# Kernel tuning notes

Measured on AMD Instinct MI355X. Metric: run time of the kernel, lower is better.

## Reference

```python
import jax, jax.numpy as jnp
import numpy as np

DIM = 768
DEC = 768
B, N = 8, 4096


def setup_inputs() -> dict:
    key = jax.random.key(0)
    ks = jax.random.split(key, 7)
    s_in = DIM ** -0.5
    s_dec = DEC ** -0.5
    return {
        "x": jax.random.normal(ks[0], (B, N, DIM), dtype=jnp.float32),
        "Wq": jax.random.normal(ks[1], (DIM, DEC), dtype=jnp.float32) * s_in,
        "Wk": jax.random.normal(ks[2], (DIM, DEC), dtype=jnp.float32) * s_in,
        "Wv": jax.random.normal(ks[3], (DIM, DEC), dtype=jnp.float32) * s_in,
        "Wr": jax.random.normal(ks[4], (DEC, DEC), dtype=jnp.float32) * s_dec,
        "alpha": jax.random.normal(ks[5], (DEC,), dtype=jnp.float32),
        "beta": jax.random.normal(ks[6], (DEC,), dtype=jnp.float32),
    }


def reference(x, Wq, Wk, Wv, Wr, alpha, beta):
    # x: [b, n, dim] -> q/k/v: [b, n, d]
    q = jnp.einsum('bni,id->bnd', x, Wq)
    k = jnp.einsum('bni,id->bnd', x, Wk)
    v = jnp.einsum('bni,id->bnd', x, Wv)
    scale = q.shape[-1] ** -0.5

    # additive attention over feature dim (softmax along d, as in source)
    alpha_w = jax.nn.softmax(q * alpha * scale, axis=-1)          # [b, n, d]
    global_q = jnp.sum(q * alpha_w, axis=1)                        # [b, d]

    p = global_q[:, None, :] * k                                   # [b, n, d]
    beta_w = jax.nn.softmax(p * beta * scale, axis=-1)             # [b, n, d]
    global_k = jnp.sum(p * beta_w, axis=1)                         # [b, d]

    kv = global_k[:, None, :] * v                                  # [b, n, d]
    out = jnp.einsum('bnd,de->bne', kv, Wr) + q                    # [b, n, d]
    return out
```

## Files before the change

kernel.cpp:

```cpp
#include <hip/hip_runtime.h>
#include <stdint.h>


#define NBATCH 8
#define SEQ 4096
#define KD 768
#define ROWS (NBATCH * SEQ)
#define NT 12

typedef __bf16 bf16x8 __attribute__((ext_vector_type(8)));
typedef float f32x4 __attribute__((ext_vector_type(4)));

__device__ __forceinline__ unsigned short f2bf(float f) {
    __bf16 h = (__bf16)f;
    return __builtin_bit_cast(unsigned short, h);
}

__device__ __forceinline__ void gload16(const void* g, void* l) {
    __builtin_amdgcn_global_load_lds((const __attribute__((address_space(1))) void*)g,
                                     (__attribute__((address_space(3))) void*)l, 16, 0, 0);
}


__global__ __launch_bounds__(256) void cvt_f32_bf16x8(const float* __restrict__ src,
                                                      unsigned short* __restrict__ dst, int n8) {
    int i = blockIdx.x * 256 + threadIdx.x;
    if (i >= n8) return;
    const float4* p = (const float4*)src + (size_t)i * 2;
    float4 a = p[0], b = p[1];
    union { unsigned short s[8]; uint4 u; } t;
    t.s[0] = f2bf(a.x); t.s[1] = f2bf(a.y); t.s[2] = f2bf(a.z); t.s[3] = f2bf(a.w);
    t.s[4] = f2bf(b.x); t.s[5] = f2bf(b.y); t.s[6] = f2bf(b.z); t.s[7] = f2bf(b.w);
    ((uint4*)dst)[i] = t.u;
}

__global__ __launch_bounds__(256) void prep_w(const float* __restrict__ Wq,
                                              const float* __restrict__ Wk,
                                              const float* __restrict__ Wr,
                                              const float* __restrict__ Wv,
                                              unsigned short* __restrict__ Wcat,
                                              unsigned short* __restrict__ WrT,
                                              unsigned short* __restrict__ Wvb) {
    __shared__ float tile[32][33];
    const int z = blockIdx.z;
    const float* src = (z == 0) ? Wq : (z == 1) ? Wk : (z == 2) ? Wr : Wv;
    unsigned short* dst = (z == 0) ? Wcat : (z == 1) ? (Wcat + KD * KD) : (z == 2) ? WrT : Wvb;
    int tx = threadIdx.x & 31, tg = threadIdx.x >> 5;
    int bi = blockIdx.x * 32, bj = blockIdx.y * 32;
    if (z == 3) {
#pragma unroll
        for (int j = 0; j < 4; ++j) {
            int r = bi + tg * 4 + j;
            dst[(size_t)r * KD + bj + tx] = f2bf(src[(size_t)r * KD + bj + tx]);
        }
        return;
    }
#pragma unroll
    for (int j = 0; j < 4; ++j) {
        int r = tg * 4 + j;
        tile[r][tx] = src[(size_t)(bi + r) * KD + bj + tx];
    }
    __syncthreads();
#pragma unroll
    for (int j = 0; j < 4; ++j) {
        int r = tg * 4 + j;
        dst[(size_t)(bj + r) * KD + bi + tx] = f2bf(tile[tx][r]);
    }
}


template <int LDC, int EPI>
__device__ __forceinline__ void gemm_core(const unsigned short* __restrict__ A,
                                          const unsigned short* __restrict__ Bp,
                                          void* __restrict__ Cout,
                                          const float* __restrict__ Wqp,
                                          int m0, int n0, char* lds) {
    const int tid = threadIdx.x;
    const int lane = tid & 63, wave = tid >> 6;
    const int wr = wave >> 1, wc = wave & 1;
    const int hi = lane >> 4, lo = lane & 15;
    char* lA = lds;
    char* lB = lds + 98304;

    f32x4 acc[4][4] = {};

    const int colb = (tid * 16) & 127;
    const int row0 = tid >> 3;
    const int sc = colb ^ ((row0 & 7) << 4);
    const size_t ldb = (size_t)KD * 2;
    const char* sAg = (const char*)A + (size_t)(m0 + row0) * ldb + sc;
    const char* sBg = (const char*)Bp + (size_t)(n0 + row0) * ldb + sc;

    const int kksel = wave & 1;
    int offA[2][4], offB[2][4];
#pragma unroll
    for (int g = 0; g < 2; ++g) {
        const int kkg = kksel ^ g;
#pragma unroll
        for (int m = 0; m < 4; ++m) {
            int ra = wr * 64 + m * 16 + lo;
            int rb = wc * 64 + m * 16 + lo;
            offA[g][m] = ra * 128 + ((kkg * 64 + hi * 16) ^ ((ra & 7) << 4));
            offB[g][m] = rb * 128 + ((kkg * 64 + hi * 16) ^ ((rb & 7) << 4));
        }
    }

#define STAGE(t)                                                              \
    {                                                                         \
        const char* ga = sAg + (t) * 128;                                     \
        const char* gb = sBg + (t) * 128;                                     \
        char* dA = lA + ((t) % 3) * 32768 + tid * 16;                         \
        char* dB = lB + ((t) % 3) * 16384 + tid * 16;                         \
        gload16(ga, dA);                                                      \
        gload16(ga + 64 * ldb, dA + 8192);                                    \
        gload16(ga + 128 * ldb, dA + 16384);                                  \
        gload16(ga + 192 * ldb, dA + 24576);                                  \
        gload16(gb, dB);                                                      \
        gload16(gb + 64 * ldb, dB + 8192);                                    \
    }

    STAGE(0);
    STAGE(1);
    asm volatile("s_waitcnt vmcnt(6)" ::: "memory");
    __builtin_amdgcn_s_barrier();
    __builtin_amdgcn_sched_barrier(0);

    for (int t = 0; t < NT; ++t) {
        if (t + 2 < NT) STAGE(t + 2);
        const char* cA = lA + (t % 3) * 32768;
        const char* cB = lB + (t % 3) * 16384;
#pragma unroll
        for (int g = 0; g < 2; ++g) {
            bf16x8 af[4], bv[4];
#pragma unroll
            for (int m = 0; m < 4; ++m) af[m] = *(const bf16x8*)(cA + offA[g][m]);
#pragma unroll
            for (int n = 0; n < 4; ++n) bv[n] = *(const bf16x8*)(cB + offB[g][n]);
            __builtin_amdgcn_s_setprio(1);
#pragma unroll
            for (int m = 0; m < 4; ++m)
#pragma unroll
                for (int n = 0; n < 4; ++n)
                    acc[m][n] = __builtin_amdgcn_mfma_f32_16x16x32_bf16(af[m], bv[n],
                                                                        acc[m][n], 0, 0, 0);
            __builtin_amdgcn_s_setprio(0);
        }
        if (t + 2 < NT)
            asm volatile("s_waitcnt vmcnt(6)" ::: "memory");
        else
            asm volatile("s_waitcnt vmcnt(0)" ::: "memory");
        __builtin_amdgcn_s_barrier();
        __builtin_amdgcn_sched_barrier(0);
    }
#undef STAGE

    const int r0 = m0 + wr * 64 + hi * 4;
    const int c0 = n0 + wc * 64 + lo;
#pragma unroll
    for (int m = 0; m < 4; ++m)
#pragma unroll
        for (int n = 0; n < 4; ++n)
#pragma unroll
            for (int r = 0; r < 4; ++r) {
                int row = r0 + m * 16 + r, col = c0 + n * 16;
                size_t idx = (size_t)row * LDC + col;
                if (EPI == 1) {
                    ((float*)Cout)[idx] = acc[m][n][r];
                } else if (EPI == 2) {
                    ((unsigned short*)Cout)[idx] =
                        f2bf(acc[m][n][r] + Wqp[(size_t)col * KD + row]);
                } else {
                    ((unsigned short*)Cout)[idx] = f2bf(acc[m][n][r]);
                }
            }
}

__device__ __forceinline__ int xcd_swz(int bid, int nwg) {
    int cpx = nwg >> 3;
    return (bid & 7) * cpx + (bid >> 3);
}

__global__ __launch_bounds__(512) void gemm_qk(const unsigned short* __restrict__ xb,
                                               const unsigned short* __restrict__ Wcat,
                                               unsigned short* __restrict__ C) {
    __shared__ char lds[147456];
    int wg = xcd_swz(blockIdx.y * gridDim.x + blockIdx.x, gridDim.x * gridDim.y);
    gemm_core<1536, 0>(xb, Wcat, C, nullptr, (wg / 12) * 256, (wg % 12) * 128, lds);
}

__global__ __launch_bounds__(512) void gemm_w3(const unsigned short* __restrict__ WrS,
                                               const unsigned short* __restrict__ Wvb,
                                               const float* __restrict__ Wq,
                                               unsigned short* __restrict__ W3T) {
    __shared__ char lds[147456];
    const int b = blockIdx.z;
    gemm_core<KD, 2>(WrS + (size_t)b * (KD * KD), Wvb, W3T + (size_t)b * (KD * KD), Wq,
                     blockIdx.y * 256, blockIdx.x * 128, lds);
}

__global__ __launch_bounds__(512) void gemm_out_f32(const unsigned short* __restrict__ xb,
                                                    const unsigned short* __restrict__ W3T,
                                                    float* __restrict__ out) {
    __shared__ char lds[147456];
    int wg = xcd_swz(blockIdx.y * gridDim.x + blockIdx.x, gridDim.x * gridDim.y);
    const int by = wg / 6, bx = wg % 6;
    const unsigned short* Bp = W3T + (size_t)(by >> 4) * (KD * KD);
    gemm_core<KD, 1>(xb, Bp, out, nullptr, by * 256, bx * 128, lds);
}


#define SM_SCALE 0.03608439182435161f
#define LDQK 1536

__device__ __forceinline__ void unpack12(const unsigned short* rowp, int lane, float* q) {
    uint4 u = *(const uint4*)(rowp + lane * 8);
    uint2 v = *(const uint2*)(rowp + 512 + lane * 4);
    q[0] = __uint_as_float(u.x << 16);  q[1] = __uint_as_float(u.x & 0xffff0000u);
    q[2] = __uint_as_float(u.y << 16);  q[3] = __uint_as_float(u.y & 0xffff0000u);
    q[4] = __uint_as_float(u.z << 16);  q[5] = __uint_as_float(u.z & 0xffff0000u);
    q[6] = __uint_as_float(u.w << 16);  q[7] = __uint_as_float(u.w & 0xffff0000u);
    q[8] = __uint_as_float(v.x << 16);  q[9] = __uint_as_float(v.x & 0xffff0000u);
    q[10] = __uint_as_float(v.y << 16); q[11] = __uint_as_float(v.y & 0xffff0000u);
}

__device__ __forceinline__ void load12f(const float* base, int lane, float* o) {
    const float4* p0 = (const float4*)(base + lane * 8);
    float4 x0 = p0[0], x1 = p0[1];
    float4 x2 = *(const float4*)(base + 512 + lane * 4);
    o[0] = x0.x; o[1] = x0.y; o[2] = x0.z; o[3] = x0.w;
    o[4] = x1.x; o[5] = x1.y; o[6] = x1.z; o[7] = x1.w;
    o[8] = x2.x; o[9] = x2.y; o[10] = x2.z; o[11] = x2.w;
}

__device__ __forceinline__ void block_partial_store(float* acc, int lane, int wave,
                                                    float* part_dst) {
    __shared__ float buf[4][KD];
#pragma unroll
    for (int j = 0; j < 8; ++j) buf[wave][lane * 8 + j] = acc[j];
#pragma unroll
    for (int j = 0; j < 4; ++j) buf[wave][512 + lane * 4 + j] = acc[8 + j];
    __syncthreads();
#pragma unroll
    for (int d = threadIdx.x; d < KD; d += 256)
        part_dst[d] = buf[0][d] + buf[1][d] + buf[2][d] + buf[3][d];
}

__global__ __launch_bounds__(256) void reduce_gq_s1(const unsigned short* __restrict__ qk,
                                                    const float* __restrict__ alpha,
                                                    float* __restrict__ part) {
    const int b = blockIdx.y;
    const int lane = threadIdx.x & 63, wave = threadIdx.x >> 6;
    float al[12];
    load12f(alpha, lane, al);
    float acc[12];
#pragma unroll
    for (int j = 0; j < 12; ++j) acc[j] = 0.f;
    const int row0 = b * SEQ + blockIdx.x * 64 + wave * 16;
#pragma unroll 2
    for (int rr = 0; rr < 16; ++rr) {
        const unsigned short* rowp = qk + (size_t)(row0 + rr) * LDQK;
        float q[12], t[12];
        unpack12(rowp, lane, q);
        float mx = -1e30f;
#pragma unroll
        for (int j = 0; j < 12; ++j) { t[j] = q[j] * al[j] * SM_SCALE; mx = fmaxf(mx, t[j]); }
#pragma unroll
        for (int s = 32; s > 0; s >>= 1) mx = fmaxf(mx, __shfl_xor(mx, s));
        float sum = 0.f, e[12];
#pragma unroll
        for (int j = 0; j < 12; ++j) { e[j] = __expf(t[j] - mx); sum += e[j]; }
#pragma unroll
        for (int s = 32; s > 0; s >>= 1) sum += __shfl_xor(sum, s);
        float inv = 1.f / sum;
#pragma unroll
        for (int j = 0; j < 12; ++j) acc[j] += q[j] * e[j] * inv;
    }
    block_partial_store(acc, lane, wave, part + ((size_t)b * 64 + blockIdx.x) * KD);
}

__global__ __launch_bounds__(256) void reduce_gk_s1(const unsigned short* __restrict__ qk,
                                                    const float* __restrict__ part1,
                                                    const float* __restrict__ beta,
                                                    float* __restrict__ part) {
    __shared__ float sgq[KD];
    const int b = blockIdx.y;
    const int lane = threadIdx.x & 63, wave = threadIdx.x >> 6;
    {
        const float* p = part1 + (size_t)b * 64 * KD;
#pragma unroll
        for (int j = 0; j < 3; ++j) {
            int d = threadIdx.x + j * 256;
            float s = 0.f;
#pragma unroll 8
            for (int i = 0; i < 64; ++i) s += p[(size_t)i * KD + d];
            sgq[d] = s;
        }
    }
    __syncthreads();
    float bt[12], gv[12];
    load12f(beta, lane, bt);
#pragma unroll
    for (int j = 0; j < 8; ++j) gv[j] = sgq[lane * 8 + j];
#pragma unroll
    for (int j = 0; j < 4; ++j) gv[8 + j] = sgq[512 + lane * 4 + j];
    float acc[12];
#pragma unroll
    for (int j = 0; j < 12; ++j) acc[j] = 0.f;
    const int row0 = b * SEQ + blockIdx.x * 64 + wave * 16;
#pragma unroll 2
    for (int rr = 0; rr < 16; ++rr) {
        const unsigned short* rowp = qk + (size_t)(row0 + rr) * LDQK + KD;
        float k[12], p[12], t[12];
        unpack12(rowp, lane, k);
        float mx = -1e30f;
#pragma unroll
        for (int j = 0; j < 12; ++j) {
            p[j] = gv[j] * k[j];
            t[j] = p[j] * bt[j] * SM_SCALE;
            mx = fmaxf(mx, t[j]);
        }
#pragma unroll
        for (int s = 32; s > 0; s >>= 1) mx = fmaxf(mx, __shfl_xor(mx, s));
        float sum = 0.f, e[12];
#pragma unroll
        for (int j = 0; j < 12; ++j) { e[j] = __expf(t[j] - mx); sum += e[j]; }
#pragma unroll
        for (int s = 32; s > 0; s >>= 1) sum += __shfl_xor(sum, s);
        float inv = 1.f / sum;
#pragma unroll
        for (int j = 0; j < 12; ++j) acc[j] += p[j] * e[j] * inv;
    }
    block_partial_store(acc, lane, wave, part + ((size_t)b * 64 + blockIdx.x) * KD);
}

__global__ __launch_bounds__(256) void sum_scale(const float* __restrict__ part2,
                                                 const unsigned short* __restrict__ WrT,
                                                 unsigned short* __restrict__ WrS) {
    __shared__ float sgk[KD];
    const int b = blockIdx.y;
    {
        const float* p = part2 + (size_t)b * 64 * KD;
#pragma unroll
        for (int j = 0; j < 3; ++j) {
            int d = threadIdx.x + j * 256;
            float s = 0.f;
#pragma unroll 8
            for (int i = 0; i < 64; ++i) s += p[(size_t)i * KD + d];
            sgk[d] = s;
        }
    }
    __syncthreads();
    const int e0 = blockIdx.x * 32;
    unsigned short* dst = WrS + (size_t)b * (KD * KD);
#pragma unroll
    for (int c = 0; c < 12; ++c) {
        int idx = c * 256 + threadIdx.x;
        int row = e0 + (idx / 96);
        int col = (idx % 96) * 8;
        uint4 w = *(const uint4*)(WrT + (size_t)row * KD + col);
        union { unsigned short s[8]; uint4 u; } o;
        o.s[0] = f2bf(__uint_as_float(w.x << 16) * sgk[col + 0]);
        o.s[1] = f2bf(__uint_as_float(w.x & 0xffff0000u) * sgk[col + 1]);
        o.s[2] = f2bf(__uint_as_float(w.y << 16) * sgk[col + 2]);
        o.s[3] = f2bf(__uint_as_float(w.y & 0xffff0000u) * sgk[col + 3]);
        o.s[4] = f2bf(__uint_as_float(w.z << 16) * sgk[col + 4]);
        o.s[5] = f2bf(__uint_as_float(w.z & 0xffff0000u) * sgk[col + 5]);
        o.s[6] = f2bf(__uint_as_float(w.w << 16) * sgk[col + 6]);
        o.s[7] = f2bf(__uint_as_float(w.w & 0xffff0000u) * sgk[col + 7]);
        *(uint4*)(dst + (size_t)row * KD + col) = o.u;
    }
}


extern "C" void kernel_launch(void* const* d_in, const int* in_sizes, int n_in,
                              void* d_out, int out_size, void* d_ws, size_t ws_size,
                              hipStream_t stream) {
    const float* x     = (const float*)d_in[0];
    const float* Wq    = (const float*)d_in[1];
    const float* Wk    = (const float*)d_in[2];
    const float* Wv    = (const float*)d_in[3];
    const float* Wr    = (const float*)d_in[4];
    const float* alpha = (const float*)d_in[5];
    const float* beta  = (const float*)d_in[6];
    float* out = (float*)d_out;
    char* ws = (char*)d_ws;

    unsigned short* xb   = (unsigned short*)(ws);
    unsigned short* qk   = (unsigned short*)(ws + 50331648);
    unsigned short* Wcat = (unsigned short*)(ws + 150994944);
    unsigned short* WrT  = (unsigned short*)(ws + 153354240);
    unsigned short* Wvb  = (unsigned short*)(ws + 154533888);
    unsigned short* WrS  = (unsigned short*)(ws + 155713536);
    unsigned short* W3T  = (unsigned short*)(ws + 165150720);
    float* part1 = (float*)(ws + 174637056);
    float* part2 = (float*)(ws + 176209920);

    cvt_f32_bf16x8<<<12288, 256, 0, stream>>>(x, xb, (ROWS * KD) / 8);
    prep_w<<<dim3(24, 24, 4), 256, 0, stream>>>(Wq, Wk, Wr, Wv, Wcat, WrT, Wvb);

    gemm_qk<<<dim3(12, 128), 512, 0, stream>>>(xb, Wcat, qk);
    reduce_gq_s1<<<dim3(64, NBATCH), 256, 0, stream>>>(qk, alpha, part1);
    reduce_gk_s1<<<dim3(64, NBATCH), 256, 0, stream>>>(qk, part1, beta, part2);

    sum_scale<<<dim3(24, NBATCH), 256, 0, stream>>>(part2, WrT, WrS);
    gemm_w3<<<dim3(6, 3, NBATCH), 512, 0, stream>>>(WrS, Wvb, Wq, W3T);
    gemm_out_f32<<<dim3(6, 128), 512, 0, stream>>>(xb, W3T, out);
}
```

Measured before the change: 393.5 us.

## Enlarge GEMM tiles to 256x256 with double buffering and fuse prep kernels

The shared GEMM core moves from 256x128 tiles with a three-stage LDS ring to 256x256 tiles with a two-stage double buffer. Each wave now computes 128x64, which raises MFMA work per LDS load and halves the block count of every GEMM. The goal is better operand reuse and less global traffic for B. In exchange each wave holds twice as many accumulator registers, the pipeline is one stage shallower, and it waits with vmcnt(0) every iteration. The x conversion and weight-prep kernels are also merged into one launch to save a kernel launch.

```diff
diff --git a/kernel.cpp b/kernel.cpp
--- a/kernel.cpp
+++ b/kernel.cpp
@@ -22,31 +22,33 @@
 }
 
 
-__global__ __launch_bounds__(256) void cvt_f32_bf16x8(const float* __restrict__ src,
-                                                      unsigned short* __restrict__ dst, int n8) {
-    int i = blockIdx.x * 256 + threadIdx.x;
-    if (i >= n8) return;
-    const float4* p = (const float4*)src + (size_t)i * 2;
-    float4 a = p[0], b = p[1];
-    union { unsigned short s[8]; uint4 u; } t;
-    t.s[0] = f2bf(a.x); t.s[1] = f2bf(a.y); t.s[2] = f2bf(a.z); t.s[3] = f2bf(a.w);
-    t.s[4] = f2bf(b.x); t.s[5] = f2bf(b.y); t.s[6] = f2bf(b.z); t.s[7] = f2bf(b.w);
-    ((uint4*)dst)[i] = t.u;
-}
-
-__global__ __launch_bounds__(256) void prep_w(const float* __restrict__ Wq,
-                                              const float* __restrict__ Wk,
-                                              const float* __restrict__ Wr,
-                                              const float* __restrict__ Wv,
-                                              unsigned short* __restrict__ Wcat,
-                                              unsigned short* __restrict__ WrT,
-                                              unsigned short* __restrict__ Wvb) {
+__global__ __launch_bounds__(256) void cvt_prep(const float* __restrict__ x,
+                                                const float* __restrict__ Wq,
+                                                const float* __restrict__ Wk,
+                                                const float* __restrict__ Wr,
+                                                const float* __restrict__ Wv,
+                                                unsigned short* __restrict__ xb,
+                                                unsigned short* __restrict__ Wcat,
+                                                unsigned short* __restrict__ WrT,
+                                                unsigned short* __restrict__ Wvb) {
     __shared__ float tile[32][33];
-    const int z = blockIdx.z;
+    const int bid = blockIdx.x;
+    if (bid < 12288) {
+        int i = bid * 256 + threadIdx.x;
+        const float4* p = (const float4*)x + (size_t)i * 2;
+        float4 a = p[0], b = p[1];
+        union { unsigned short s[8]; uint4 u; } t;
+        t.s[0] = f2bf(a.x); t.s[1] = f2bf(a.y); t.s[2] = f2bf(a.z); t.s[3] = f2bf(a.w);
+        t.s[4] = f2bf(b.x); t.s[5] = f2bf(b.y); t.s[6] = f2bf(b.z); t.s[7] = f2bf(b.w);
+        ((uint4*)xb)[i] = t.u;
+        return;
+    }
+    const int idx = bid - 12288;
+    const int z = idx / 576, rem = idx % 576;
     const float* src = (z == 0) ? Wq : (z == 1) ? Wk : (z == 2) ? Wr : Wv;
     unsigned short* dst = (z == 0) ? Wcat : (z == 1) ? (Wcat + KD * KD) : (z == 2) ? WrT : Wvb;
-    int tx = threadIdx.x & 31, tg = threadIdx.x >> 5;
-    int bi = blockIdx.x * 32, bj = blockIdx.y * 32;
+    const int tx = threadIdx.x & 31, tg = threadIdx.x >> 5;
+    const int bi = (rem / 24) * 32, bj = (rem % 24) * 32;
     if (z == 3) {
 #pragma unroll
         for (int j = 0; j < 4; ++j) {
@@ -70,38 +72,37 @@
 
 
 template <int LDC, int EPI>
-__device__ __forceinline__ void gemm_core(const unsigned short* __restrict__ A,
-                                          const unsigned short* __restrict__ Bp,
-                                          void* __restrict__ Cout,
-                                          const float* __restrict__ Wqp,
-                                          int m0, int n0, char* lds) {
+__device__ __forceinline__ void gemm_core256(const unsigned short* __restrict__ A,
+                                             const unsigned short* __restrict__ Bp,
+                                             void* __restrict__ Cout,
+                                             const float* __restrict__ Wqp,
+                                             int m0, int n0, char* lds) {
     const int tid = threadIdx.x;
     const int lane = tid & 63, wave = tid >> 6;
-    const int wr = wave >> 1, wc = wave & 1;
+    const int wr = wave >> 2, wc = wave & 3;
     const int hi = lane >> 4, lo = lane & 15;
-    char* lA = lds;
-    char* lB = lds + 98304;
-
-    f32x4 acc[4][4] = {};
-
-    const int colb = (tid * 16) & 127;
+
+    f32x4 acc[8][4] = {};
+
+    const int colb = (tid & 7) * 16;
     const int row0 = tid >> 3;
     const int sc = colb ^ ((row0 & 7) << 4);
     const size_t ldb = (size_t)KD * 2;
     const char* sAg = (const char*)A + (size_t)(m0 + row0) * ldb + sc;
     const char* sBg = (const char*)Bp + (size_t)(n0 + row0) * ldb + sc;
 
-    const int kksel = wave & 1;
-    int offA[2][4], offB[2][4];
-#pragma unroll
-    for (int g = 0; g < 2; ++g) {
-        const int kkg = kksel ^ g;
-#pragma unroll
-        for (int m = 0; m < 4; ++m) {
-            int ra = wr * 64 + m * 16 + lo;
-            int rb = wc * 64 + m * 16 + lo;
-            offA[g][m] = ra * 128 + ((kkg * 64 + hi * 16) ^ ((ra & 7) << 4));
-            offB[g][m] = rb * 128 + ((kkg * 64 + hi * 16) ^ ((rb & 7) << 4));
+    int offA[2][8], offB[2][4];
+#pragma unroll
+    for (int kk = 0; kk < 2; ++kk) {
+#pragma unroll
+        for (int m = 0; m < 8; ++m) {
+            int ra = wr * 128 + m * 16 + lo;
+            offA[kk][m] = ra * 128 + ((kk * 64 + hi * 16) ^ ((ra & 7) << 4));
+        }
+#pragma unroll
+        for (int n = 0; n < 4; ++n) {
+            int rb = wc * 64 + n * 16 + lo;
+            offB[kk][n] = 32768 + rb * 128 + ((kk * 64 + hi * 16) ^ ((rb & 7) << 4));
         }
     }
 
@@ -109,55 +110,54 @@
     {                                                                         \
         const char* ga = sAg + (t) * 128;                                     \
         const char* gb = sBg + (t) * 128;                                     \
-        char* dA = lA + ((t) % 3) * 32768 + tid * 16;                         \
-        char* dB = lB + ((t) % 3) * 16384 + tid * 16;                         \
+        char* dA = lds + ((t) & 1) * 65536 + tid * 16;                        \
+        char* dB = dA + 32768;                                                \
         gload16(ga, dA);                                                      \
         gload16(ga + 64 * ldb, dA + 8192);                                    \
         gload16(ga + 128 * ldb, dA + 16384);                                  \
         gload16(ga + 192 * ldb, dA + 24576);                                  \
         gload16(gb, dB);                                                      \
         gload16(gb + 64 * ldb, dB + 8192);                                    \
+        gload16(gb + 128 * ldb, dB + 16384);                                  \
+        gload16(gb + 192 * ldb, dB + 24576);                                  \
     }
 
     STAGE(0);
-    STAGE(1);
-    asm volatile("s_waitcnt vmcnt(6)" ::: "memory");
+    asm volatile("s_waitcnt vmcnt(0)" ::: "memory");
     __builtin_amdgcn_s_barrier();
     __builtin_amdgcn_sched_barrier(0);
 
     for (int t = 0; t < NT; ++t) {
-        if (t + 2 < NT) STAGE(t + 2);
-        const char* cA = lA + (t % 3) * 32768;
-        const char* cB = lB + (t % 3) * 16384;
-#pragma unroll
-        for (int g = 0; g < 2; ++g) {
-            bf16x8 af[4], bv[4];
-#pragma unroll
-            for (int m = 0; m < 4; ++m) af[m] = *(const bf16x8*)(cA + offA[g][m]);
-#pragma unroll
-            for (int n = 0; n < 4; ++n) bv[n] = *(const bf16x8*)(cB + offB[g][n]);
+        if (t + 1 < NT) STAGE(t + 1);
+        const char* cb = lds + (t & 1) * 65536;
+#pragma unroll
+        for (int kk = 0; kk < 2; ++kk) {
+            bf16x8 af[8], bv[4];
+#pragma unroll
+            for (int m = 0; m < 8; ++m) af[m] = *(const bf16x8*)(cb + offA[kk][m]);
+#pragma unroll
+            for (int n = 0; n < 4; ++n) bv[n] = *(const bf16x8*)(cb + offB[kk][n]);
             __builtin_amdgcn_s_setprio(1);
 #pragma unroll
-            for (int m = 0; m < 4; ++m)
+            for (int m = 0; m < 8; ++m)
 #pragma unroll
                 for (int n = 0; n < 4; ++n)
                     acc[m][n] = __builtin_amdgcn_mfma_f32_16x16x32_bf16(af[m], bv[n],
                                                                         acc[m][n], 0, 0, 0);
             __builtin_amdgcn_s_setprio(0);
         }
-        if (t + 2 < NT)
-            asm volatile("s_waitcnt vmcnt(6)" ::: "memory");
-        else
+        if (t + 1 < NT) {
             asm volatile("s_waitcnt vmcnt(0)" ::: "memory");
-        __builtin_amdgcn_s_barrier();
-        __builtin_amdgcn_sched_barrier(0);
+            __builtin_amdgcn_s_barrier();
+            __builtin_amdgcn_sched_barrier(0);
+        }
     }
 #undef STAGE
 
-    const int r0 = m0 + wr * 64 + hi * 4;
+    const int r0 = m0 + wr * 128 + hi * 4;
     const int c0 = n0 + wc * 64 + lo;
 #pragma unroll
-    for (int m = 0; m < 4; ++m)
+    for (int m = 0; m < 8; ++m)
 #pragma unroll
         for (int n = 0; n < 4; ++n)
 #pragma unroll
@@ -180,32 +180,32 @@
     return (bid & 7) * cpx + (bid >> 3);
 }
 
-__global__ __launch_bounds__(512) void gemm_qk(const unsigned short* __restrict__ xb,
-                                               const unsigned short* __restrict__ Wcat,
-                                               unsigned short* __restrict__ C) {
-    __shared__ char lds[147456];
+__global__ __launch_bounds__(512, 2) void gemm_qk(const unsigned short* __restrict__ xb,
+                                                  const unsigned short* __restrict__ Wcat,
+                                                  unsigned short* __restrict__ C) {
+    __shared__ char lds[131072];
     int wg = xcd_swz(blockIdx.y * gridDim.x + blockIdx.x, gridDim.x * gridDim.y);
-    gemm_core<1536, 0>(xb, Wcat, C, nullptr, (wg / 12) * 256, (wg % 12) * 128, lds);
-}
-
-__global__ __launch_bounds__(512) void gemm_w3(const unsigned short* __restrict__ WrS,
-                                               const unsigned short* __restrict__ Wvb,
-                                               const float* __restrict__ Wq,
-                                               unsigned short* __restrict__ W3T) {
-    __shared__ char lds[147456];
+    gemm_core256<1536, 0>(xb, Wcat, C, nullptr, (wg / 6) * 256, (wg % 6) * 256, lds);
+}
+
+__global__ __launch_bounds__(512, 2) void gemm_w3(const unsigned short* __restrict__ WrS,
+                                                  const unsigned short* __restrict__ Wvb,
+                                                  const float* __restrict__ Wq,
+                                                  unsigned short* __restrict__ W3T) {
+    __shared__ char lds[131072];
     const int b = blockIdx.z;
-    gemm_core<KD, 2>(WrS + (size_t)b * (KD * KD), Wvb, W3T + (size_t)b * (KD * KD), Wq,
-                     blockIdx.y * 256, blockIdx.x * 128, lds);
-}
-
-__global__ __launch_bounds__(512) void gemm_out_f32(const unsigned short* __restrict__ xb,
-                                                    const unsigned short* __restrict__ W3T,
-                                                    float* __restrict__ out) {
-    __shared__ char lds[147456];
+    gemm_core256<KD, 2>(WrS + (size_t)b * (KD * KD), Wvb, W3T + (size_t)b * (KD * KD), Wq,
+                        blockIdx.y * 256, blockIdx.x * 256, lds);
+}
+
+__global__ __launch_bounds__(512, 2) void gemm_out_f32(const unsigned short* __restrict__ xb,
+                                                       const unsigned short* __restrict__ W3T,
+                                                       float* __restrict__ out) {
+    __shared__ char lds[131072];
     int wg = xcd_swz(blockIdx.y * gridDim.x + blockIdx.x, gridDim.x * gridDim.y);
-    const int by = wg / 6, bx = wg % 6;
+    const int by = wg / 3, bx = wg % 3;
     const unsigned short* Bp = W3T + (size_t)(by >> 4) * (KD * KD);
-    gemm_core<KD, 1>(xb, Bp, out, nullptr, by * 256, bx * 128, lds);
+    gemm_core256<KD, 1>(xb, Bp, out, nullptr, by * 256, bx * 256, lds);
 }
 
 
@@ -378,10 +378,12 @@
     const float* x     = (const float*)d_in[0];
     const float* Wq    = (const float*)d_in[1];
     const float* Wk    = (const float*)d_in[2];
+    const float* Wr    = (const float*)d_in[3 - 1];
     const float* Wv    = (const float*)d_in[3];
-    const float* Wr    = (const float*)d_in[4];
+    const float* Wr_   = (const float*)d_in[4];
     const float* alpha = (const float*)d_in[5];
     const float* beta  = (const float*)d_in[6];
+    (void)Wr;
     float* out = (float*)d_out;
     char* ws = (char*)d_ws;
 
@@ -395,14 +397,13 @@
     float* part1 = (float*)(ws + 174637056);
     float* part2 = (float*)(ws + 176209920);
 
-    cvt_f32_bf16x8<<<12288, 256, 0, stream>>>(x, xb, (ROWS * KD) / 8);
-    prep_w<<<dim3(24, 24, 4), 256, 0, stream>>>(Wq, Wk, Wr, Wv, Wcat, WrT, Wvb);
-
-    gemm_qk<<<dim3(12, 128), 512, 0, stream>>>(xb, Wcat, qk);
+    cvt_prep<<<14592, 256, 0, stream>>>(x, Wq, Wk, Wr_, Wv, xb, Wcat, WrT, Wvb);
+
+    gemm_qk<<<dim3(6, 128), 512, 0, stream>>>(xb, Wcat, qk);
     reduce_gq_s1<<<dim3(64, NBATCH), 256, 0, stream>>>(qk, alpha, part1);
     reduce_gk_s1<<<dim3(64, NBATCH), 256, 0, stream>>>(qk, part1, beta, part2);
 
     sum_scale<<<dim3(24, NBATCH), 256, 0, stream>>>(part2, WrT, WrS);
-    gemm_w3<<<dim3(6, 3, NBATCH), 512, 0, stream>>>(WrS, Wvb, Wq, W3T);
-    gemm_out_f32<<<dim3(6, 128), 512, 0, stream>>>(xb, W3T, out);
-}
+    gemm_w3<<<dim3(3, 3, NBATCH), 512, 0, stream>>>(WrS, Wvb, Wq, W3T);
+    gemm_out_f32<<<dim3(3, 128), 512, 0, stream>>>(xb, W3T, out);
+}
```

Result: no change. 388.0 us (-1.4%).
